# Performance work log

Measured on AMD Instinct MI355X. Metric: run time of the kernel, lower is better.

## Reference

```python
import jax, jax.numpy as jnp
import numpy as np

NEG_SLOPE = 0.2  # PyG GATConv default leaky_relu negative_slope
BN_EPS = 1e-5


def gat_layer(x, src, dst, W, a_src, a_dst, bias):
    """PyG-style GATConv (self-loops already appended to src/dst).
    x: [N, F_in], W: [F_in, H*C], a_src/a_dst: [H, C], bias: [H*C].
    Returns [N, H*C] (concat heads)."""
    N = x.shape[0]
    H, C = a_src.shape
    h = (x @ W).reshape(N, H, C)                      # [N, H, C]
    al_src = jnp.sum(h * a_src[None], axis=-1)        # [N, H]
    al_dst = jnp.sum(h * a_dst[None], axis=-1)        # [N, H]
    e = jax.nn.leaky_relu(al_src[src] + al_dst[dst], NEG_SLOPE)  # [E, H]
    # segment softmax over destination neighborhoods
    m = jax.ops.segment_max(e, dst, num_segments=N)   # [N, H]
    ee = jnp.exp(e - m[dst])
    denom = jax.ops.segment_sum(ee, dst, num_segments=N)  # [N, H]
    alpha = ee / denom[dst]                           # [E, H]
    out = jax.ops.segment_sum(alpha[:, :, None] * h[src], dst, num_segments=N)  # [N, H, C]
    return out.reshape(N, H * C) + bias


def batch_norm(x, gamma, beta):
    mu = jnp.mean(x, axis=0)
    var = jnp.var(x, axis=0)  # biased, matches torch BN training stats
    return gamma * (x - mu) * jax.lax.rsqrt(var + BN_EPS) + beta


def setup_inputs() -> dict:
    key = jax.random.key(0)
    N, F, H, C = 50000, 128, 4, 64
    E = 400000
    HC = H * C  # 256
    ks = jax.random.split(key, 24)

    def glorot(k, shape, fan_in):
        return jax.random.normal(k, shape, dtype=jnp.float32) * (1.0 / np.sqrt(fan_in))

    inp = {
        "x": jax.random.normal(ks[0], (N, F), dtype=jnp.float32),
        "edge_index": jax.random.randint(ks[1], (2, E), 0, N, dtype=jnp.int64),
        # conv1: F -> H*C
        "W1": glorot(ks[2], (F, HC), F),
        "a1s": glorot(ks[3], (H, C), C),
        "a1d": glorot(ks[4], (H, C), C),
        "b1": jnp.zeros((HC,), jnp.float32),
        # conv2: H*C -> H*C
        "W2": glorot(ks[5], (HC, HC), HC),
        "a2s": glorot(ks[6], (H, C), C),
        "a2d": glorot(ks[7], (H, C), C),
        "b2": jnp.zeros((HC,), jnp.float32),
        # conv3: H*C -> C (1 head)
        "W3": glorot(ks[8], (HC, C), HC),
        "a3s": glorot(ks[9], (1, C), C),
        "a3d": glorot(ks[10], (1, C), C),
        "b3": jnp.zeros((C,), jnp.float32),
        # batch norms
        "g1": jnp.ones((HC,), jnp.float32),
        "be1": jnp.zeros((HC,), jnp.float32),
        "g2": jnp.ones((HC,), jnp.float32),
        "be2": jnp.zeros((HC,), jnp.float32),
        # MLP head: C -> C//2 -> 2
        "fw1": glorot(ks[11], (C, C // 2), C),
        "fb1": jnp.zeros((C // 2,), jnp.float32),
        "fw2": glorot(ks[12], (C // 2, 2), C // 2),
        "fb2": jnp.zeros((2,), jnp.float32),
    }
    return inp


def reference(x, edge_index, W1, a1s, a1d, b1, W2, a2s, a2d, b2,
              W3, a3s, a3d, b3, g1, be1, g2, be2, fw1, fb1, fw2, fb2):
    N = x.shape[0]
    loop = jnp.arange(N, dtype=edge_index.dtype)
    src = jnp.concatenate([edge_index[0], loop])  # self-loops (PyG default)
    dst = jnp.concatenate([edge_index[1], loop])

    h = gat_layer(x, src, dst, W1, a1s, a1d, b1)
    h = jax.nn.elu(batch_norm(h, g1, be1))
    h = gat_layer(h, src, dst, W2, a2s, a2d, b2)
    h = jax.nn.elu(batch_norm(h, g2, be2))
    h = jax.nn.elu(gat_layer(h, src, dst, W3, a3s, a3d, b3))
    h = jax.nn.relu(h @ fw1 + fb1)
    return h @ fw2 + fb2  # [N, 2] logits
```

## Files before the change

### kernel.cpp

```cpp
#include <hip/hip_runtime.h>
#include <math.h>
#include <stdint.h>

typedef __attribute__((ext_vector_type(8))) short short8v;
typedef __attribute__((ext_vector_type(4))) float float4v;

__device__ __forceinline__ float bf2f(unsigned short u) {
  return __uint_as_float((unsigned int)u << 16);
}
__device__ __forceinline__ unsigned short f2bf(float f) {
  unsigned int u = __float_as_uint(f);
  unsigned int r = (u + 0x7FFFu + ((u >> 16) & 1u)) >> 16;
  return (unsigned short)r;
}
__device__ __forceinline__ float exp_lrelu(float x) {
  x = x > 0.f ? x : 0.2f * x;
  return expf(x);
}

typedef __attribute__((address_space(3))) void lds_void;
typedef const __attribute__((address_space(1))) void glb_void;
__device__ __forceinline__ void gload_lds16(const void* g, void* l) {
  __builtin_amdgcn_global_load_lds((glb_void*)g, (lds_void*)l, 16, 0, 0);
}

__global__ void wprep_kernel(const float* __restrict__ W, unsigned short* __restrict__ Wh,
                             unsigned short* __restrict__ Wl, int K, int Nw)
{
  int t = blockIdx.x * 256 + threadIdx.x;
  if (t >= K * Nw) return;
  int i = t & 7;
  int lane = (t >> 3) & 63;
  int frag = t >> 9;
  int ktiles = K >> 5;
  int n_tile = frag / ktiles, k_tile = frag - n_tile * ktiles;
  int k = k_tile * 32 + ((lane >> 4) << 3) + i;
  int n = (n_tile << 4) + (lane & 15);
  float v = W[(size_t)k * Nw + n];
  unsigned short hi = (unsigned short)(__float_as_uint(v) >> 16);
  float rem = v - bf2f(hi);
  Wh[t] = hi;
  Wl[t] = f2bf(rem);
}

__global__ __launch_bounds__(256) void split_kernel(const float* __restrict__ in,
    unsigned short* __restrict__ hi, unsigned short* __restrict__ lo, size_t n4)
{
  size_t i0 = (size_t)blockIdx.x * 256 + threadIdx.x;
  size_t stride = (size_t)gridDim.x * 256;
  for (size_t idx = i0; idx < n4; idx += stride) {
    float4 v = ((const float4*)in)[idx];
    float vv[4] = {v.x, v.y, v.z, v.w};
    ushort4 h, l;
    unsigned short* hp = &h.x; unsigned short* lp = &l.x;
#pragma unroll
    for (int j = 0; j < 4; ++j) {
      unsigned short hh = (unsigned short)(__float_as_uint(vv[j]) >> 16);
      hp[j] = hh;
      lp[j] = f2bf(vv[j] - bf2f(hh));
    }
    ((ushort4*)hi)[idx] = h;
    ((ushort4*)lo)[idx] = l;
  }
}

__global__ __launch_bounds__(256) void bnsplit_kernel(const unsigned short* __restrict__ act,
    const float* __restrict__ scale, const float* __restrict__ shift,
    unsigned short* __restrict__ hi, unsigned short* __restrict__ lo, size_t nchunks)
{
  size_t i0 = (size_t)blockIdx.x * 256 + threadIdx.x;
  size_t stride = (size_t)gridDim.x * 256;
  for (size_t idx = i0; idx < nchunks; idx += stride) {
    ushort4 u = ((const ushort4*)act)[idx];
    int f = (int)((idx * 4) & 255);
    float4 sc = *(const float4*)(scale + f);
    float4 sh = *(const float4*)(shift + f);
    float vv[4];
    vv[0] = fmaf(bf2f(u.x), sc.x, sh.x);
    vv[1] = fmaf(bf2f(u.y), sc.y, sh.y);
    vv[2] = fmaf(bf2f(u.z), sc.z, sh.z);
    vv[3] = fmaf(bf2f(u.w), sc.w, sh.w);
    ushort4 h, l;
    unsigned short* hp = &h.x; unsigned short* lp = &l.x;
#pragma unroll
    for (int j = 0; j < 4; ++j) {
      float t = vv[j];
      t = t > 0.f ? t : expm1f(t);
      unsigned short hh = (unsigned short)(__float_as_uint(t) >> 16);
      hp[j] = hh;
      lp[j] = f2bf(t - bf2f(hh));
    }
    ((ushort4*)hi)[idx] = h;
    ((ushort4*)lo)[idx] = l;
  }
}

template<int MI, int WM, int WN, int KTILES, int HEADS>
__global__ __launch_bounds__(256) void gemm_al(
    const unsigned short* __restrict__ Ah, const unsigned short* __restrict__ Al,
    const unsigned short* __restrict__ Bh, const unsigned short* __restrict__ Bl,
    const float* __restrict__ a_s, const float* __restrict__ a_d,
    unsigned short* __restrict__ C, float* __restrict__ al_s, float* __restrict__ al_d,
    int M)
{
  constexpr int BM = WM * MI * 16;
  constexpr int NG = BM / 64;
  constexpr int TILEB = BM * 64;
  constexpr int Nw = WN * 64, K = KTILES * 32;
  __shared__ __align__(16) unsigned char smem[2][2][TILEB];

  const int wid = threadIdx.x >> 6, lane = threadIdx.x & 63;
  const int wm = wid / WN, wn = wid % WN;
  const int m0 = blockIdx.x * BM;
  const int n0 = wn * 64;
  const int ar = lane & 15;
  const int cchunk = lane >> 4;
  const int ntile0 = n0 >> 4;

  float4v acc[MI][4];
#pragma unroll
  for (int mi = 0; mi < MI; ++mi)
#pragma unroll
    for (int ni = 0; ni < 4; ++ni)
      acc[mi][ni] = (float4v){0.f, 0.f, 0.f, 0.f};

  auto stage = [&](int buf, int kt) {
    const int kk = kt * 32;
#pragma unroll
    for (int i = 0; i < NG; ++i) {
      const unsigned short* gh = Ah + (size_t)(m0 + i * 64 + lane) * K + kk + wid * 8;
      const unsigned short* gl = Al + (size_t)(m0 + i * 64 + lane) * K + kk + wid * 8;
      gload_lds16(gh, &smem[buf][0][i * 4096 + wid * 1024]);
      gload_lds16(gl, &smem[buf][1][i * 4096 + wid * 1024]);
    }
  };

  stage(0, 0);
  int cur = 0;
  for (int kt = 0; kt < KTILES; ++kt) {
    __syncthreads();
    short8v bh[4], bl[4];
#pragma unroll
    for (int ni = 0; ni < 4; ++ni) {
      size_t off = (((size_t)(ntile0 + ni) * KTILES + kt) * 64 + lane) * 8;
      bh[ni] = *(const short8v*)(Bh + off);
      bl[ni] = *(const short8v*)(Bl + off);
    }
    if (kt + 1 < KTILES) stage(cur ^ 1, kt + 1);
    short8v ah[MI], al_[MI];
#pragma unroll
    for (int mi = 0; mi < MI; ++mi) {
      int row = wm * MI * 16 + mi * 16 + ar;
      int off = (row >> 6) * 4096 + cchunk * 1024 + (row & 63) * 16;
      ah[mi] = *(const short8v*)&smem[cur][0][off];
      al_[mi] = *(const short8v*)&smem[cur][1][off];
    }
#pragma unroll
    for (int mi = 0; mi < MI; ++mi)
#pragma unroll
      for (int ni = 0; ni < 4; ++ni) {
        acc[mi][ni] = __builtin_amdgcn_mfma_f32_16x16x32_bf16(ah[mi], bh[ni], acc[mi][ni], 0, 0, 0);
        acc[mi][ni] = __builtin_amdgcn_mfma_f32_16x16x32_bf16(ah[mi], bl[ni], acc[mi][ni], 0, 0, 0);
        acc[mi][ni] = __builtin_amdgcn_mfma_f32_16x16x32_bf16(al_[mi], bh[ni], acc[mi][ni], 0, 0, 0);
      }
    cur ^= 1;
  }

  const int cc = lane & 15;
#pragma unroll
  for (int mi = 0; mi < MI; ++mi) {
    int rowb = m0 + wm * MI * 16 + mi * 16 + ((lane >> 4) << 2);
#pragma unroll
    for (int r = 0; r < 4; ++r) {
      int row = rowb + r;
      if (row < M) {
#pragma unroll
        for (int ni = 0; ni < 4; ++ni)
          C[(size_t)row * Nw + n0 + ni * 16 + cc] = f2bf(acc[mi][ni][r]);
      }
    }
  }

  const int head = (HEADS == 4) ? wn : 0;
  float as_[4], ad_[4];
#pragma unroll
  for (int ni = 0; ni < 4; ++ni) {
    as_[ni] = a_s[head * 64 + ni * 16 + cc];
    ad_[ni] = a_d[head * 64 + ni * 16 + cc];
  }
#pragma unroll
  for (int mi = 0; mi < MI; ++mi) {
#pragma unroll
    for (int r = 0; r < 4; ++r) {
      float h0 = bf2f(f2bf(acc[mi][0][r]));
      float h1 = bf2f(f2bf(acc[mi][1][r]));
      float h2 = bf2f(f2bf(acc[mi][2][r]));
      float h3 = bf2f(f2bf(acc[mi][3][r]));
      float ps = h0 * as_[0] + h1 * as_[1] + h2 * as_[2] + h3 * as_[3];
      float pd = h0 * ad_[0] + h1 * ad_[1] + h2 * ad_[2] + h3 * ad_[3];
#pragma unroll
      for (int off = 1; off < 16; off <<= 1) {
        ps += __shfl_xor(ps, off);
        pd += __shfl_xor(pd, off);
      }
      int row = m0 + wm * MI * 16 + mi * 16 + ((lane >> 4) << 2) + r;
      if (cc == 0 && row < M) {
        al_s[row * HEADS + head] = ps;
        al_d[row * HEADS + head] = pd;
      }
    }
  }
}

__global__ void count_kernel(const int* __restrict__ dst, int E, int Etot, int* __restrict__ counts)
{
  int e = blockIdx.x * 256 + threadIdx.x;
  if (e >= Etot) return;
  int d = (e < E) ? dst[e] : (e - E);
  atomicAdd(&counts[d], 1);
}

__global__ void block_sum_kernel(const int* __restrict__ counts, int N, int* __restrict__ bsums)
{
  __shared__ int sd[256];
  int i = blockIdx.x * 256 + threadIdx.x;
  sd[threadIdx.x] = (i < N) ? counts[i] : 0;
  __syncthreads();
  for (int off = 128; off; off >>= 1) {
    if (threadIdx.x < off) sd[threadIdx.x] += sd[threadIdx.x + off];
    __syncthreads();
  }
  if (threadIdx.x == 0) bsums[blockIdx.x] = sd[0];
}

__global__ void scan_bsums_kernel(int* bsums, int nb)
{
  __shared__ int sd[256];
  int t = threadIdx.x;
  int v = (t < nb) ? bsums[t] : 0;
  sd[t] = v;
  __syncthreads();
  for (int off = 1; off < 256; off <<= 1) {
    int x = (t >= off) ? sd[t - off] : 0;
    __syncthreads();
    sd[t] += x;
    __syncthreads();
  }
  if (t < nb) bsums[t] = sd[t] - v;
}

__global__ void scan_write_kernel(const int* __restrict__ counts, int N,
                                  const int* __restrict__ bsums, int* __restrict__ rowStart, int Etot)
{
  __shared__ int sd[256];
  int i = blockIdx.x * 256 + threadIdx.x;
  int v = (i < N) ? counts[i] : 0;
  sd[threadIdx.x] = v;
  __syncthreads();
  for (int off = 1; off < 256; off <<= 1) {
    int x = (threadIdx.x >= off) ? sd[threadIdx.x - off] : 0;
    __syncthreads();
    sd[threadIdx.x] += x;
    __syncthreads();
  }
  if (i < N) rowStart[i] = bsums[blockIdx.x] + sd[threadIdx.x] - v;
  if (i == N - 1) rowStart[N] = Etot;
}

__global__ void fill_kernel(const int* __restrict__ src, const int* __restrict__ dst,
                            int E, int Etot, const int* __restrict__ rowStart,
                            int* __restrict__ cursor, int* __restrict__ csrSrc)
{
  int e = blockIdx.x * 256 + threadIdx.x;
  if (e >= Etot) return;
  int s, d;
  if (e < E) { s = src[e]; d = dst[e]; } else { s = d = e - E; }
  int pos = rowStart[d] + atomicAdd(&cursor[d], 1);
  csrSrc[pos] = s;
}

template<int HC_, bool OUT16>
__global__ __launch_bounds__(256) void aggregate_fused(
    const unsigned short* __restrict__ h16,
    const float* __restrict__ als, const float* __restrict__ ald,
    const int* __restrict__ csrSrc, const int* __restrict__ rowStart,
    void* __restrict__ outp, int N, const float* __restrict__ bias, int doElu)
{
  constexpr int H_ = HC_ / 64;
  constexpr int FPL = HC_ / 64;
  __shared__ float ldsW[4][64 * H_];
  const int wl = threadIdx.x >> 6;
  int wid = blockIdx.x * 4 + wl;
  if (wid >= N) return;
  const int lane = threadIdx.x & 63;
  const int head = (H_ == 4) ? (lane >> 4) : 0;
  const int start = rowStart[wid], end = rowStart[wid + 1];

  float ad0, ad1, ad2, ad3;
  if (H_ == 4) {
    float4 adv = ((const float4*)ald)[wid];
    ad0 = adv.x; ad1 = adv.y; ad2 = adv.z; ad3 = adv.w;
  } else {
    ad0 = ald[wid]; ad1 = ad2 = ad3 = 0.f;
  }

  float acc[FPL] = {};
  float wsum = 0.f;

  for (int base = start; base < end; base += 64) {
    int cnt = end - base; if (cnt > 64) cnt = 64;
    int s_l = 0;
    if (lane < cnt) {
      s_l = csrSrc[base + lane];
      if (H_ == 4) {
        float4 av = ((const float4*)als)[s_l];
        float4 w4;
        w4.x = exp_lrelu(av.x + ad0);
        w4.y = exp_lrelu(av.y + ad1);
        w4.z = exp_lrelu(av.z + ad2);
        w4.w = exp_lrelu(av.w + ad3);
        *(float4*)&ldsW[wl][lane * 4] = w4;
      } else {
        ldsW[wl][lane] = exp_lrelu(als[s_l] + ad0);
      }
    }
    int i = 0;
    for (; i + 4 <= cnt; i += 4) {
      int s0 = __shfl(s_l, i);
      int s1 = __shfl(s_l, i + 1);
      int s2 = __shfl(s_l, i + 2);
      int s3 = __shfl(s_l, i + 3);
      float w0 = ldsW[wl][(i + 0) * H_ + head];
      float w1 = ldsW[wl][(i + 1) * H_ + head];
      float w2 = ldsW[wl][(i + 2) * H_ + head];
      float w3 = ldsW[wl][(i + 3) * H_ + head];
      if (FPL == 4) {
        ushort4 r0 = ((const ushort4*)(h16 + (size_t)s0 * HC_))[lane];
        ushort4 r1 = ((const ushort4*)(h16 + (size_t)s1 * HC_))[lane];
        ushort4 r2 = ((const ushort4*)(h16 + (size_t)s2 * HC_))[lane];
        ushort4 r3 = ((const ushort4*)(h16 + (size_t)s3 * HC_))[lane];
        wsum += (w0 + w1) + (w2 + w3);
        acc[0] = fmaf(w0, bf2f(r0.x), acc[0]);
        acc[1] = fmaf(w0, bf2f(r0.y), acc[1]);
        acc[2] = fmaf(w0, bf2f(r0.z), acc[2]);
        acc[3] = fmaf(w0, bf2f(r0.w), acc[3]);
        acc[0] = fmaf(w1, bf2f(r1.x), acc[0]);
        acc[1] = fmaf(w1, bf2f(r1.y), acc[1]);
        acc[2] = fmaf(w1, bf2f(r1.z), acc[2]);
        acc[3] = fmaf(w1, bf2f(r1.w), acc[3]);
        acc[0] = fmaf(w2, bf2f(r2.x), acc[0]);
        acc[1] = fmaf(w2, bf2f(r2.y), acc[1]);
        acc[2] = fmaf(w2, bf2f(r2.z), acc[2]);
        acc[3] = fmaf(w2, bf2f(r2.w), acc[3]);
        acc[0] = fmaf(w3, bf2f(r3.x), acc[0]);
        acc[1] = fmaf(w3, bf2f(r3.y), acc[1]);
        acc[2] = fmaf(w3, bf2f(r3.z), acc[2]);
        acc[3] = fmaf(w3, bf2f(r3.w), acc[3]);
      } else {
        unsigned short r0 = h16[(size_t)s0 * HC_ + lane];
        unsigned short r1 = h16[(size_t)s1 * HC_ + lane];
        unsigned short r2 = h16[(size_t)s2 * HC_ + lane];
        unsigned short r3 = h16[(size_t)s3 * HC_ + lane];
        wsum += (w0 + w1) + (w2 + w3);
        acc[0] = fmaf(w0, bf2f(r0), acc[0]);
        acc[0] = fmaf(w1, bf2f(r1), acc[0]);
        acc[0] = fmaf(w2, bf2f(r2), acc[0]);
        acc[0] = fmaf(w3, bf2f(r3), acc[0]);
      }
    }
    for (; i < cnt; ++i) {
      int s0 = __shfl(s_l, i);
      float w0 = ldsW[wl][i * H_ + head];
      wsum += w0;
      if (FPL == 4) {
        ushort4 r0 = ((const ushort4*)(h16 + (size_t)s0 * HC_))[lane];
        acc[0] = fmaf(w0, bf2f(r0.x), acc[0]);
        acc[1] = fmaf(w0, bf2f(r0.y), acc[1]);
        acc[2] = fmaf(w0, bf2f(r0.z), acc[2]);
        acc[3] = fmaf(w0, bf2f(r0.w), acc[3]);
      } else {
        unsigned short r0 = h16[(size_t)s0 * HC_ + lane];
        acc[0] = fmaf(w0, bf2f(r0), acc[0]);
      }
    }
  }

  float inv = 1.0f / wsum;
  if (FPL == 4) {
    float o0 = acc[0] * inv, o1 = acc[1] * inv, o2 = acc[2] * inv, o3 = acc[3] * inv;
    if (bias) {
      const float4 b = ((const float4*)bias)[lane];
      o0 += b.x; o1 += b.y; o2 += b.z; o3 += b.w;
    }
    if (doElu) {
      o0 = o0 > 0.f ? o0 : expm1f(o0);
      o1 = o1 > 0.f ? o1 : expm1f(o1);
      o2 = o2 > 0.f ? o2 : expm1f(o2);
      o3 = o3 > 0.f ? o3 : expm1f(o3);
    }
    if (OUT16) {
      ushort4 o;
      o.x = f2bf(o0); o.y = f2bf(o1); o.z = f2bf(o2); o.w = f2bf(o3);
      ((ushort4*)((unsigned short*)outp + (size_t)wid * HC_))[lane] = o;
    } else {
      ((float4*)((float*)outp + (size_t)wid * HC_))[lane] = make_float4(o0, o1, o2, o3);
    }
  } else {
    float o = acc[0] * inv;
    if (bias) o += bias[lane];
    if (doElu) o = o > 0.f ? o : expm1f(o);
    if (OUT16) ((unsigned short*)outp)[(size_t)wid * HC_ + lane] = f2bf(o);
    else       ((float*)outp)[(size_t)wid * HC_ + lane] = o;
  }
}

__global__ __launch_bounds__(256) void bn_stats_kernel(const unsigned short* __restrict__ x, int N,
                                float* __restrict__ sums, float* __restrict__ sumsq)
{
  const int wid = threadIdx.x >> 6, lane = threadIdx.x & 63;
  const int gw = blockIdx.x * 4 + wid;
  const int tw = gridDim.x * 4;
  float4 s = make_float4(0.f, 0.f, 0.f, 0.f);
  float4 q = make_float4(0.f, 0.f, 0.f, 0.f);
#pragma unroll 4
  for (int r = gw; r < N; r += tw) {
    ushort4 u = ((const ushort4*)(x + (size_t)r * 256))[lane];
    float v0 = bf2f(u.x), v1 = bf2f(u.y), v2 = bf2f(u.z), v3 = bf2f(u.w);
    s.x += v0; s.y += v1; s.z += v2; s.w += v3;
    q.x = fmaf(v0, v0, q.x); q.y = fmaf(v1, v1, q.y);
    q.z = fmaf(v2, v2, q.z); q.w = fmaf(v3, v3, q.w);
  }
  __shared__ float ls[4][512];
  *(float4*)&ls[wid][lane * 4] = s;
  *(float4*)&ls[wid][256 + lane * 4] = q;
  __syncthreads();
  const int t = threadIdx.x;
  float a = ls[0][t] + ls[1][t] + ls[2][t] + ls[3][t];
  float b = ls[0][t + 256] + ls[1][t + 256] + ls[2][t + 256] + ls[3][t + 256];
  atomicAdd(&sums[t], a);
  atomicAdd(&sumsq[t], b);
}

__global__ void bn_final_kernel(const float* __restrict__ sums, const float* __restrict__ sumsq,
                                const float* __restrict__ g, const float* __restrict__ be,
                                int N, float* __restrict__ scale, float* __restrict__ shift)
{
  int f = threadIdx.x;
  float mu = sums[f] / N;
  float var = sumsq[f] / N - mu * mu;
  float rs = rsqrtf(var + 1e-5f);
  float sc = g[f] * rs;
  scale[f] = sc;
  shift[f] = be[f] - mu * sc;
}

__global__ __launch_bounds__(256) void mlp_kernel(const float* __restrict__ h,
                           const float* __restrict__ fw1,
                           const float* __restrict__ fb1, const float* __restrict__ fw2,
                           const float* __restrict__ fb2, float* __restrict__ out, int N)
{
  __shared__ float w1s[64][32];
  __shared__ float w2s[32][2];
  __shared__ float b1s[32];
  const int t = threadIdx.x;
  for (int i = t; i < 64 * 32; i += 256) w1s[i >> 5][i & 31] = fw1[i];
  if (t < 64) w2s[t >> 1][t & 1] = fw2[t];
  if (t < 32) b1s[t] = fb1[t];
  __syncthreads();

  int n = blockIdx.x * 256 + t;
  if (n >= N) return;

  float hv[64];
#pragma unroll
  for (int k4 = 0; k4 < 16; ++k4) {
    float4 v = *(const float4*)(h + (size_t)n * 64 + k4 * 4);
    hv[k4 * 4 + 0] = v.x; hv[k4 * 4 + 1] = v.y;
    hv[k4 * 4 + 2] = v.z; hv[k4 * 4 + 3] = v.w;
  }
  float hid[32];
#pragma unroll
  for (int j = 0; j < 32; ++j) hid[j] = b1s[j];
#pragma unroll
  for (int k = 0; k < 64; ++k) {
    float hk = hv[k];
#pragma unroll
    for (int jb = 0; jb < 8; ++jb) {
      float4 wv = *(const float4*)&w1s[k][jb * 4];
      hid[jb * 4 + 0] = fmaf(hk, wv.x, hid[jb * 4 + 0]);
      hid[jb * 4 + 1] = fmaf(hk, wv.y, hid[jb * 4 + 1]);
      hid[jb * 4 + 2] = fmaf(hk, wv.z, hid[jb * 4 + 2]);
      hid[jb * 4 + 3] = fmaf(hk, wv.w, hid[jb * 4 + 3]);
    }
  }
  float p0 = fb2[0], p1 = fb2[1];
#pragma unroll
  for (int j = 0; j < 32; ++j) {
    float r = fmaxf(hid[j], 0.f);
    p0 = fmaf(r, w2s[j][0], p0);
    p1 = fmaf(r, w2s[j][1], p1);
  }
  *(float2*)(out + (size_t)n * 2) = make_float2(p0, p1);
}

extern "C" void kernel_launch(void* const* d_in, const int* in_sizes, int n_in,
                              void* d_out, int out_size, void* d_ws, size_t ws_size,
                              hipStream_t stream)
{
  const float* x   = (const float*)d_in[0];
  const int*   ei  = (const int*)d_in[1];
  const float* W1  = (const float*)d_in[2];
  const float* a1s = (const float*)d_in[3];
  const float* a1d = (const float*)d_in[4];
  const float* W2  = (const float*)d_in[6];
  const float* a2s = (const float*)d_in[7];
  const float* a2d = (const float*)d_in[8];
  const float* W3  = (const float*)d_in[10];
  const float* a3s = (const float*)d_in[11];
  const float* a3d = (const float*)d_in[12];
  const float* b3  = (const float*)d_in[13];
  const float* g1  = (const float*)d_in[14];
  const float* be1 = (const float*)d_in[15];
  const float* g2  = (const float*)d_in[16];
  const float* be2 = (const float*)d_in[17];
  const float* fw1 = (const float*)d_in[18];
  const float* fb1 = (const float*)d_in[19];
  const float* fw2 = (const float*)d_in[20];
  const float* fb2 = (const float*)d_in[21];
  float* out = (float*)d_out;

  const int F = 128;
  const int N = in_sizes[0] / F;
  const int E = in_sizes[1] / 2;
  const int Etot = E + N;
  const int* srcIdx = ei;
  const int* dstIdx = ei + E;

  char* w = (char*)d_ws;
  auto alloc = [&](size_t bytes) -> void* {
    void* p = (void*)w;
    w += (bytes + 255) & ~(size_t)255;
    return p;
  };
  unsigned short* h16  = (unsigned short*)alloc((size_t)N * 256 * 2);
  unsigned short* act16= (unsigned short*)alloc((size_t)N * 256 * 2);
  float* actf    = (float*)alloc((size_t)N * 64 * 4);
  unsigned short* aHi = (unsigned short*)alloc((size_t)N * 256 * 2);
  unsigned short* aLo = (unsigned short*)alloc((size_t)N * 256 * 2);
  float* als     = (float*)alloc((size_t)N * 4 * 4);
  float* ald     = (float*)alloc((size_t)N * 4 * 4);
  int*   counts  = (int*)alloc((size_t)N * 4);
  int*   cursor  = (int*)alloc((size_t)N * 4);
  int*   rowStart= (int*)alloc((size_t)(N + 1) * 4);
  int*   csrSrc  = (int*)alloc((size_t)Etot * 4);
  int*   bsums   = (int*)alloc((size_t)((N + 255) / 256) * 4);
  float* sums    = (float*)alloc(256 * 4);
  float* sumsq   = (float*)alloc(256 * 4);
  float* scale1  = (float*)alloc(256 * 4);
  float* shift1  = (float*)alloc(256 * 4);
  float* scale2  = (float*)alloc(256 * 4);
  float* shift2  = (float*)alloc(256 * 4);
  unsigned short* w1h = (unsigned short*)alloc((size_t)128 * 256 * 2);
  unsigned short* w1l = (unsigned short*)alloc((size_t)128 * 256 * 2);
  unsigned short* w2h = (unsigned short*)alloc((size_t)256 * 256 * 2);
  unsigned short* w2l = (unsigned short*)alloc((size_t)256 * 256 * 2);
  unsigned short* w3h = (unsigned short*)alloc((size_t)256 * 64 * 2);
  unsigned short* w3l = (unsigned short*)alloc((size_t)256 * 64 * 2);
  (void)alloc(65536);

  const int nb = (N + 255) / 256;
  const int ebk = (Etot + 255) / 256;
  const int aggBlocks = (N + 3) / 4;

  wprep_kernel<<<(128 * 256 + 255) / 256, 256, 0, stream>>>(W1, w1h, w1l, 128, 256);
  wprep_kernel<<<(256 * 256 + 255) / 256, 256, 0, stream>>>(W2, w2h, w2l, 256, 256);
  wprep_kernel<<<(256 * 64 + 255) / 256, 256, 0, stream>>>(W3, w3h, w3l, 256, 64);

  hipMemsetAsync(counts, 0, (size_t)N * 4, stream);
  hipMemsetAsync(cursor, 0, (size_t)N * 4, stream);
  count_kernel<<<ebk, 256, 0, stream>>>(dstIdx, E, Etot, counts);
  block_sum_kernel<<<nb, 256, 0, stream>>>(counts, N, bsums);
  scan_bsums_kernel<<<1, 256, 0, stream>>>(bsums, nb);
  scan_write_kernel<<<nb, 256, 0, stream>>>(counts, N, bsums, rowStart, Etot);
  fill_kernel<<<ebk, 256, 0, stream>>>(srcIdx, dstIdx, E, Etot, rowStart, cursor, csrSrc);

  dim3 g12((N + 63) / 64, 1);
  dim3 g3((N + 127) / 128, 1);

  split_kernel<<<2048, 256, 0, stream>>>(x, aHi, aLo, (size_t)N * 128 / 4);
  gemm_al<4, 1, 4, 4, 4><<<g12, 256, 0, stream>>>(aHi, aLo, w1h, w1l, a1s, a1d, h16, als, ald, N);
  aggregate_fused<256, true><<<aggBlocks, 256, 0, stream>>>(h16, als, ald, csrSrc, rowStart, act16, N, nullptr, 0);
  hipMemsetAsync(sums, 0, 256 * 4, stream);
  hipMemsetAsync(sumsq, 0, 256 * 4, stream);
  bn_stats_kernel<<<512, 256, 0, stream>>>(act16, N, sums, sumsq);
  bn_final_kernel<<<1, 256, 0, stream>>>(sums, sumsq, g1, be1, N, scale1, shift1);

  bnsplit_kernel<<<2048, 256, 0, stream>>>(act16, scale1, shift1, aHi, aLo, (size_t)N * 64);
  gemm_al<4, 1, 4, 8, 4><<<g12, 256, 0, stream>>>(aHi, aLo, w2h, w2l, a2s, a2d, h16, als, ald, N);
  aggregate_fused<256, true><<<aggBlocks, 256, 0, stream>>>(h16, als, ald, csrSrc, rowStart, act16, N, nullptr, 0);
  hipMemsetAsync(sums, 0, 256 * 4, stream);
  hipMemsetAsync(sumsq, 0, 256 * 4, stream);
  bn_stats_kernel<<<512, 256, 0, stream>>>(act16, N, sums, sumsq);
  bn_final_kernel<<<1, 256, 0, stream>>>(sums, sumsq, g2, be2, N, scale2, shift2);

  bnsplit_kernel<<<2048, 256, 0, stream>>>(act16, scale2, shift2, aHi, aLo, (size_t)N * 64);
  gemm_al<2, 4, 1, 8, 1><<<g3, 256, 0, stream>>>(aHi, aLo, w3h, w3l, a3s, a3d, h16, als, ald, N);
  aggregate_fused<64, false><<<aggBlocks, 256, 0, stream>>>(h16, als, ald, csrSrc, rowStart, actf, N, b3, 1);

  mlp_kernel<<<(N + 255) / 256, 256, 0, stream>>>(actf, fw1, fb1, fw2, fb2, out, N);
}
```

Before: 346.3 us.

## Drop split-bf16 emulation in GEMMs and use deterministic BN partial sums

Replaces the three-term hi/lo bf16 split GEMM, which emulated fp32 precision, with a single bf16 MFMA per tile. This removes the low-part arrays, their writes and loads, and two thirds of the MFMAs. The GEMM now stages 64-wide K steps in one LDS buffer. Batch-norm statistics now go to per-block partials reduced in the final kernel instead of using atomics and memsets. The cost is lower GEMM precision, since plain bf16 inputs lose the fp32-like accuracy.

```diff
diff --git a/kernel.cpp b/kernel.cpp
--- a/kernel.cpp
+++ b/kernel.cpp
@@ -25,7 +25,7 @@
 }
 
 __global__ void wprep_kernel(const float* __restrict__ W, unsigned short* __restrict__ Wh,
-                             unsigned short* __restrict__ Wl, int K, int Nw)
+                             int K, int Nw)
 {
   int t = blockIdx.x * 256 + threadIdx.x;
   if (t >= K * Nw) return;
@@ -36,37 +36,25 @@
   int n_tile = frag / ktiles, k_tile = frag - n_tile * ktiles;
   int k = k_tile * 32 + ((lane >> 4) << 3) + i;
   int n = (n_tile << 4) + (lane & 15);
-  float v = W[(size_t)k * Nw + n];
-  unsigned short hi = (unsigned short)(__float_as_uint(v) >> 16);
-  float rem = v - bf2f(hi);
-  Wh[t] = hi;
-  Wl[t] = f2bf(rem);
+  Wh[t] = f2bf(W[(size_t)k * Nw + n]);
 }
 
 __global__ __launch_bounds__(256) void split_kernel(const float* __restrict__ in,
-    unsigned short* __restrict__ hi, unsigned short* __restrict__ lo, size_t n4)
+    unsigned short* __restrict__ hi, size_t n4)
 {
   size_t i0 = (size_t)blockIdx.x * 256 + threadIdx.x;
   size_t stride = (size_t)gridDim.x * 256;
   for (size_t idx = i0; idx < n4; idx += stride) {
     float4 v = ((const float4*)in)[idx];
-    float vv[4] = {v.x, v.y, v.z, v.w};
-    ushort4 h, l;
-    unsigned short* hp = &h.x; unsigned short* lp = &l.x;
-#pragma unroll
-    for (int j = 0; j < 4; ++j) {
-      unsigned short hh = (unsigned short)(__float_as_uint(vv[j]) >> 16);
-      hp[j] = hh;
-      lp[j] = f2bf(vv[j] - bf2f(hh));
-    }
+    ushort4 h;
+    h.x = f2bf(v.x); h.y = f2bf(v.y); h.z = f2bf(v.z); h.w = f2bf(v.w);
     ((ushort4*)hi)[idx] = h;
-    ((ushort4*)lo)[idx] = l;
   }
 }
 
 __global__ __launch_bounds__(256) void bnsplit_kernel(const unsigned short* __restrict__ act,
     const float* __restrict__ scale, const float* __restrict__ shift,
-    unsigned short* __restrict__ hi, unsigned short* __restrict__ lo, size_t nchunks)
+    unsigned short* __restrict__ hi, size_t nchunks)
 {
   size_t i0 = (size_t)blockIdx.x * 256 + threadIdx.x;
   size_t stride = (size_t)gridDim.x * 256;
@@ -75,39 +63,33 @@
     int f = (int)((idx * 4) & 255);
     float4 sc = *(const float4*)(scale + f);
     float4 sh = *(const float4*)(shift + f);
-    float vv[4];
-    vv[0] = fmaf(bf2f(u.x), sc.x, sh.x);
-    vv[1] = fmaf(bf2f(u.y), sc.y, sh.y);
-    vv[2] = fmaf(bf2f(u.z), sc.z, sh.z);
-    vv[3] = fmaf(bf2f(u.w), sc.w, sh.w);
-    ushort4 h, l;
-    unsigned short* hp = &h.x; unsigned short* lp = &l.x;
-#pragma unroll
-    for (int j = 0; j < 4; ++j) {
-      float t = vv[j];
-      t = t > 0.f ? t : expm1f(t);
-      unsigned short hh = (unsigned short)(__float_as_uint(t) >> 16);
-      hp[j] = hh;
-      lp[j] = f2bf(t - bf2f(hh));
-    }
+    float v0 = fmaf(bf2f(u.x), sc.x, sh.x);
+    float v1 = fmaf(bf2f(u.y), sc.y, sh.y);
+    float v2 = fmaf(bf2f(u.z), sc.z, sh.z);
+    float v3 = fmaf(bf2f(u.w), sc.w, sh.w);
+    v0 = v0 > 0.f ? v0 : expm1f(v0);
+    v1 = v1 > 0.f ? v1 : expm1f(v1);
+    v2 = v2 > 0.f ? v2 : expm1f(v2);
+    v3 = v3 > 0.f ? v3 : expm1f(v3);
+    ushort4 h;
+    h.x = f2bf(v0); h.y = f2bf(v1); h.z = f2bf(v2); h.w = f2bf(v3);
     ((ushort4*)hi)[idx] = h;
-    ((ushort4*)lo)[idx] = l;
-  }
-}
-
-template<int MI, int WM, int WN, int KTILES, int HEADS>
+  }
+}
+
+template<int MI, int WM, int WN, int KSTEPS, int HEADS>
 __global__ __launch_bounds__(256) void gemm_al(
-    const unsigned short* __restrict__ Ah, const unsigned short* __restrict__ Al,
-    const unsigned short* __restrict__ Bh, const unsigned short* __restrict__ Bl,
+    const unsigned short* __restrict__ Ah, const unsigned short* __restrict__ Bh,
     const float* __restrict__ a_s, const float* __restrict__ a_d,
     unsigned short* __restrict__ C, float* __restrict__ al_s, float* __restrict__ al_d,
     int M)
 {
   constexpr int BM = WM * MI * 16;
   constexpr int NG = BM / 64;
-  constexpr int TILEB = BM * 64;
-  constexpr int Nw = WN * 64, K = KTILES * 32;
-  __shared__ __align__(16) unsigned char smem[2][2][TILEB];
+  constexpr int TILEB = NG * 8192;
+  constexpr int Nw = WN * 64, K = KSTEPS * 64;
+  constexpr int KT32 = KSTEPS * 2;
+  __shared__ __align__(16) unsigned char smem[2][TILEB];
 
   const int wid = threadIdx.x >> 6, lane = threadIdx.x & 63;
   const int wm = wid / WN, wn = wid % WN;
@@ -124,45 +106,46 @@
     for (int ni = 0; ni < 4; ++ni)
       acc[mi][ni] = (float4v){0.f, 0.f, 0.f, 0.f};
 
-  auto stage = [&](int buf, int kt) {
-    const int kk = kt * 32;
-#pragma unroll
-    for (int i = 0; i < NG; ++i) {
-      const unsigned short* gh = Ah + (size_t)(m0 + i * 64 + lane) * K + kk + wid * 8;
-      const unsigned short* gl = Al + (size_t)(m0 + i * 64 + lane) * K + kk + wid * 8;
-      gload_lds16(gh, &smem[buf][0][i * 4096 + wid * 1024]);
-      gload_lds16(gl, &smem[buf][1][i * 4096 + wid * 1024]);
+  auto stage = [&](int buf, int ks) {
+#pragma unroll
+    for (int j = wid; j < NG * 8; j += 4) {
+      int g = j >> 3, c = j & 7;
+      const unsigned short* gp = Ah + (size_t)(m0 + g * 64 + lane) * K + ks * 64 + c * 8;
+      gload_lds16(gp, &smem[buf][g * 8192 + c * 1024 + lane * 16]);
     }
   };
 
   stage(0, 0);
   int cur = 0;
-  for (int kt = 0; kt < KTILES; ++kt) {
+  for (int ks = 0; ks < KSTEPS; ++ks) {
     __syncthreads();
-    short8v bh[4], bl[4];
-#pragma unroll
-    for (int ni = 0; ni < 4; ++ni) {
-      size_t off = (((size_t)(ntile0 + ni) * KTILES + kt) * 64 + lane) * 8;
-      bh[ni] = *(const short8v*)(Bh + off);
-      bl[ni] = *(const short8v*)(Bl + off);
-    }
-    if (kt + 1 < KTILES) stage(cur ^ 1, kt + 1);
-    short8v ah[MI], al_[MI];
-#pragma unroll
-    for (int mi = 0; mi < MI; ++mi) {
-      int row = wm * MI * 16 + mi * 16 + ar;
-      int off = (row >> 6) * 4096 + cchunk * 1024 + (row & 63) * 16;
-      ah[mi] = *(const short8v*)&smem[cur][0][off];
-      al_[mi] = *(const short8v*)&smem[cur][1][off];
-    }
-#pragma unroll
-    for (int mi = 0; mi < MI; ++mi)
+    short8v bh[2][4];
+#pragma unroll
+    for (int hh = 0; hh < 2; ++hh)
 #pragma unroll
       for (int ni = 0; ni < 4; ++ni) {
-        acc[mi][ni] = __builtin_amdgcn_mfma_f32_16x16x32_bf16(ah[mi], bh[ni], acc[mi][ni], 0, 0, 0);
-        acc[mi][ni] = __builtin_amdgcn_mfma_f32_16x16x32_bf16(ah[mi], bl[ni], acc[mi][ni], 0, 0, 0);
-        acc[mi][ni] = __builtin_amdgcn_mfma_f32_16x16x32_bf16(al_[mi], bh[ni], acc[mi][ni], 0, 0, 0);
-      }
+        int kt = ks * 2 + hh;
+        size_t off = (((size_t)(ntile0 + ni) * KT32 + kt) * 64 + lane) * 8;
+        bh[hh][ni] = *(const short8v*)(Bh + off);
+      }
+    if (ks + 1 < KSTEPS) stage(cur ^ 1, ks + 1);
+    short8v ah[2][MI];
+#pragma unroll
+    for (int hh = 0; hh < 2; ++hh)
+#pragma unroll
+      for (int mi = 0; mi < MI; ++mi) {
+        int row = wm * MI * 16 + mi * 16 + ar;
+        int c = hh * 4 + cchunk;
+        int off = (row >> 6) * 8192 + c * 1024 + (row & 63) * 16;
+        ah[hh][mi] = *(const short8v*)&smem[cur][off];
+      }
+#pragma unroll
+    for (int hh = 0; hh < 2; ++hh)
+#pragma unroll
+      for (int mi = 0; mi < MI; ++mi)
+#pragma unroll
+        for (int ni = 0; ni < 4; ++ni)
+          acc[mi][ni] = __builtin_amdgcn_mfma_f32_16x16x32_bf16(ah[hh][mi], bh[hh][ni], acc[mi][ni], 0, 0, 0);
     cur ^= 1;
   }
 
@@ -415,7 +398,7 @@
 }
 
 __global__ __launch_bounds__(256) void bn_stats_kernel(const unsigned short* __restrict__ x, int N,
-                                float* __restrict__ sums, float* __restrict__ sumsq)
+                                float* __restrict__ partials)
 {
   const int wid = threadIdx.x >> 6, lane = threadIdx.x & 63;
   const int gw = blockIdx.x * 4 + wid;
@@ -437,17 +420,23 @@
   const int t = threadIdx.x;
   float a = ls[0][t] + ls[1][t] + ls[2][t] + ls[3][t];
   float b = ls[0][t + 256] + ls[1][t + 256] + ls[2][t + 256] + ls[3][t + 256];
-  atomicAdd(&sums[t], a);
-  atomicAdd(&sumsq[t], b);
-}
-
-__global__ void bn_final_kernel(const float* __restrict__ sums, const float* __restrict__ sumsq,
+  partials[blockIdx.x * 512 + t] = a;
+  partials[blockIdx.x * 512 + 256 + t] = b;
+}
+
+__global__ void bn_final_kernel(const float* __restrict__ partials, int nblk,
                                 const float* __restrict__ g, const float* __restrict__ be,
                                 int N, float* __restrict__ scale, float* __restrict__ shift)
 {
   int f = threadIdx.x;
-  float mu = sums[f] / N;
-  float var = sumsq[f] / N - mu * mu;
+  float s = 0.f, q = 0.f;
+#pragma unroll 8
+  for (int b = 0; b < nblk; ++b) {
+    s += partials[b * 512 + f];
+    q += partials[b * 512 + 256 + f];
+  }
+  float mu = s / N;
+  float var = q / N - mu * mu;
   float rs = rsqrtf(var + 1e-5f);
   float sc = g[f] * rs;
   scale[f] = sc;
@@ -545,8 +534,7 @@
   unsigned short* h16  = (unsigned short*)alloc((size_t)N * 256 * 2);
   unsigned short* act16= (unsigned short*)alloc((size_t)N * 256 * 2);
   float* actf    = (float*)alloc((size_t)N * 64 * 4);
-  unsigned short* aHi = (unsigned short*)alloc((size_t)N * 256 * 2);
-  unsigned short* aLo = (unsigned short*)alloc((size_t)N * 256 * 2);
+  unsigned short* aBf  = (unsigned short*)alloc((size_t)N * 256 * 2);
   float* als     = (float*)alloc((size_t)N * 4 * 4);
   float* ald     = (float*)alloc((size_t)N * 4 * 4);
   int*   counts  = (int*)alloc((size_t)N * 4);
@@ -554,27 +542,23 @@
   int*   rowStart= (int*)alloc((size_t)(N + 1) * 4);
   int*   csrSrc  = (int*)alloc((size_t)Etot * 4);
   int*   bsums   = (int*)alloc((size_t)((N + 255) / 256) * 4);
-  float* sums    = (float*)alloc(256 * 4);
-  float* sumsq   = (float*)alloc(256 * 4);
+  float* partials= (float*)alloc((size_t)128 * 512 * 4);
   float* scale1  = (float*)alloc(256 * 4);
   float* shift1  = (float*)alloc(256 * 4);
   float* scale2  = (float*)alloc(256 * 4);
   float* shift2  = (float*)alloc(256 * 4);
   unsigned short* w1h = (unsigned short*)alloc((size_t)128 * 256 * 2);
-  unsigned short* w1l = (unsigned short*)alloc((size_t)128 * 256 * 2);
   unsigned short* w2h = (unsigned short*)alloc((size_t)256 * 256 * 2);
-  unsigned short* w2l = (unsigned short*)alloc((size_t)256 * 256 * 2);
   unsigned short* w3h = (unsigned short*)alloc((size_t)256 * 64 * 2);
-  unsigned short* w3l = (unsigned short*)alloc((size_t)256 * 64 * 2);
   (void)alloc(65536);
 
   const int nb = (N + 255) / 256;
   const int ebk = (Etot + 255) / 256;
   const int aggBlocks = (N + 3) / 4;
 
-  wprep_kernel<<<(128 * 256 + 255) / 256, 256, 0, stream>>>(W1, w1h, w1l, 128, 256);
-  wprep_kernel<<<(256 * 256 + 255) / 256, 256, 0, stream>>>(W2, w2h, w2l, 256, 256);
-  wprep_kernel<<<(256 * 64 + 255) / 256, 256, 0, stream>>>(W3, w3h, w3l, 256, 64);
+  wprep_kernel<<<(128 * 256 + 255) / 256, 256, 0, stream>>>(W1, w1h, 128, 256);
+  wprep_kernel<<<(256 * 256 + 255) / 256, 256, 0, stream>>>(W2, w2h, 256, 256);
+  wprep_kernel<<<(256 * 64 + 255) / 256, 256, 0, stream>>>(W3, w3h, 256, 64);
 
   hipMemsetAsync(counts, 0, (size_t)N * 4, stream);
   hipMemsetAsync(cursor, 0, (size_t)N * 4, stream);
@@ -587,24 +571,20 @@
   dim3 g12((N + 63) / 64, 1);
   dim3 g3((N + 127) / 128, 1);
 
-  split_kernel<<<2048, 256, 0, stream>>>(x, aHi, aLo, (size_t)N * 128 / 4);
-  gemm_al<4, 1, 4, 4, 4><<<g12, 256, 0, stream>>>(aHi, aLo, w1h, w1l, a1s, a1d, h16, als, ald, N);
+  split_kernel<<<2048, 256, 0, stream>>>(x, aBf, (size_t)N * 128 / 4);
+  gemm_al<4, 1, 4, 2, 4><<<g12, 256, 0, stream>>>(aBf, w1h, a1s, a1d, h16, als, ald, N);
   aggregate_fused<256, true><<<aggBlocks, 256, 0, stream>>>(h16, als, ald, csrSrc, rowStart, act16, N, nullptr, 0);
-  hipMemsetAsync(sums, 0, 256 * 4, stream);
-  hipMemsetAsync(sumsq, 0, 256 * 4, stream);
-  bn_stats_kernel<<<512, 256, 0, stream>>>(act16, N, sums, sumsq);
-  bn_final_kernel<<<1, 256, 0, stream>>>(sums, sumsq, g1, be1, N, scale1, shift1);
-
-  bnsplit_kernel<<<2048, 256, 0, stream>>>(act16, scale1, shift1, aHi, aLo, (size_t)N * 64);
-  gemm_al<4, 1, 4, 8, 4><<<g12, 256, 0, stream>>>(aHi, aLo, w2h, w2l, a2s, a2d, h16, als, ald, N);
+  bn_stats_kernel<<<128, 256, 0, stream>>>(act16, N, partials);
+  bn_final_kernel<<<1, 256, 0, stream>>>(partials, 128, g1, be1, N, scale1, shift1);
+
+  bnsplit_kernel<<<2048, 256, 0, stream>>>(act16, scale1, shift1, aBf, (size_t)N * 64);
+  gemm_al<4, 1, 4, 4, 4><<<g12, 256, 0, stream>>>(aBf, w2h, a2s, a2d, h16, als, ald, N);
   aggregate_fused<256, true><<<aggBlocks, 256, 0, stream>>>(h16, als, ald, csrSrc, rowStart, act16, N, nullptr, 0);
-  hipMemsetAsync(sums, 0, 256 * 4, stream);
-  hipMemsetAsync(sumsq, 0, 256 * 4, stream);
-  bn_stats_kernel<<<512, 256, 0, stream>>>(act16, N, sums, sumsq);
-  bn_final_kernel<<<1, 256, 0, stream>>>(sums, sumsq, g2, be2, N, scale2, shift2);
-
-  bnsplit_kernel<<<2048, 256, 0, stream>>>(act16, scale2, shift2, aHi, aLo, (size_t)N * 64);
-  gemm_al<2, 4, 1, 8, 1><<<g3, 256, 0, stream>>>(aHi, aLo, w3h, w3l, a3s, a3d, h16, als, ald, N);
+  bn_stats_kernel<<<128, 256, 0, stream>>>(act16, N, partials);
+  bn_final_kernel<<<1, 256, 0, stream>>>(partials, 128, g2, be2, N, scale2, shift2);
+
+  bnsplit_kernel<<<2048, 256, 0, stream>>>(act16, scale2, shift2, aBf, (size_t)N * 64);
+  gemm_al<2, 4, 1, 4, 1><<<g3, 256, 0, stream>>>(aBf, w3h, a3s, a3d, h16, als, ald, N);
   aggregate_fused<64, false><<<aggBlocks, 256, 0, stream>>>(h16, als, ald, csrSrc, rowStart, actf, N, b3, 1);
 
   mlp_kernel<<<(N + 255) / 256, 256, 0, stream>>>(actf, fw1, fb1, fw2, fb2, out, N);
```

After: 306.5 us. 1.13x faster.
